# Kernel optimization log

Hardware: AMD Instinct MI355X
Metric: run time of the kernel (lower is better)

## Reference

```python
import jax, jax.numpy as jnp
import numpy as np

# SigNet forward: time-augment -> depth-3 path signature (basepoint=True, via
# Chen's identity over per-segment tensor exponentials) -> Linear. dropout p=0.

B, L, CIN, OUT = 256, 256, 8, 128
C = CIN + 1                      # +1 time channel from signatory.Augment
SIG_CH = C + C**2 + C**3         # signatory.signature_channels(C, depth=3) = 819


def setup_inputs() -> dict:
    key = jax.random.key(0)
    k1, k2, k3 = jax.random.split(key, 3)
    inp = jax.random.normal(k1, (B, L, CIN), dtype=jnp.float32)
    W = jax.random.normal(k2, (SIG_CH, OUT), dtype=jnp.float32) / np.sqrt(SIG_CH).astype(np.float32)
    b = jax.random.normal(k3, (OUT,), dtype=jnp.float32) * 0.01
    return {"inp": inp, "W": W, "b": b}


def _chen(a, bb):
    # Chen's identity for truncated tensor algebra (depth 3):
    # (a*b)_k = sum_{i+j=k} a_i (x) b_j  (with a_0 = b_0 = 1)
    a1, a2, a3 = a
    b1, b2, b3 = bb
    c1 = a1 + b1
    c2 = a2 + b2 + jnp.einsum('...i,...j->...ij', a1, b1)
    c3 = (a3 + b3
          + jnp.einsum('...ij,...k->...ijk', a2, b1)
          + jnp.einsum('...i,...jk->...ijk', a1, b2))
    return (c1, c2, c3)


def _signature_depth3(path):
    # path: [B, L, C]; basepoint=True -> prepend the zero point before diffing
    Bn, Ln, Cn = path.shape
    path = jnp.concatenate([jnp.zeros((Bn, 1, Cn), path.dtype), path], axis=1)
    dx = jnp.moveaxis(jnp.diff(path, axis=1), 1, 0)  # [L, B, C] increments
    # Tensor exponential of each linear segment: exp(dx)_k = dx^{(x)k} / k!
    e1 = dx
    e2 = 0.5 * jnp.einsum('lbi,lbj->lbij', dx, dx)
    e3 = jnp.einsum('lbij,lbk->lbijk', e2, dx) / 3.0  # = dx^(x)3 / 6
    s1, s2, s3 = jax.lax.associative_scan(_chen, (e1, e2, e3), axis=0)
    return jnp.concatenate([s1[-1].reshape(Bn, -1),
                            s2[-1].reshape(Bn, -1),
                            s3[-1].reshape(Bn, -1)], axis=-1)  # [B, SIG_CH]


def reference(inp, W, b):
    Bn, Ln, _ = inp.shape
    # signatory.Augment include_time: linspace(0,1,L) channel, placed first
    t = jnp.broadcast_to(jnp.linspace(0.0, 1.0, Ln, dtype=inp.dtype)[None, :, None], (Bn, Ln, 1))
    x = jnp.concatenate([t, inp], axis=-1)  # [B, L, C]
    y = _signature_depth3(x)
    return y @ W + b  # dropout p=0 is identity
```

## Files before the change

kernel.cpp:

```cpp
#include <hip/hip_runtime.h>


#define ROWF   260
#define NCHUNK 16
#define TPC    27
#define ASTRIDE 29
#define PART_S2_OFF (NCHUNK * TPC * ASTRIDE)
#define UNION_FLOATS (PART_S2_OFF + NCHUNK * 81)

__global__ __launch_bounds__(512) void signet_fwd(
    const float* __restrict__ inp,
    const float* __restrict__ Wg,
    const float* __restrict__ bias,
    float* __restrict__ out)
{
    __shared__ float sig[820];
    __shared__ __align__(16) float u[UNION_FLOATS];

    float* Wt = u;
    float* Dt = u + 9 * ROWF;

    const int tid = threadIdx.x;
    const int b   = blockIdx.x;

    {
        const int t = tid & 255;
        const float* rc = inp + (size_t)b * 2048 + (size_t)t * 8;
        if (tid < 256) {
            float4 c0 = *(const float4*)rc;
            float4 p0 = make_float4(0.f, 0.f, 0.f, 0.f);
            float  tp = 0.f;
            if (t > 0) { p0 = *(const float4*)(rc - 8); tp = (float)(t - 1) * (1.0f / 255.0f); }
            float cur[5] = { (float)t * (1.0f / 255.0f), c0.x, c0.y, c0.z, c0.w };
            float prv[5] = { tp, p0.x, p0.y, p0.z, p0.w };
            #pragma unroll
            for (int c = 0; c < 5; ++c) {
                const float d = cur[c] - prv[c];
                Dt[c * ROWF + t] = d;
                Wt[c * ROWF + t] = prv[c] + 0.5f * d;
            }
        } else {
            float4 c1 = *(const float4*)(rc + 4);
            float4 p1 = make_float4(0.f, 0.f, 0.f, 0.f);
            if (t > 0) p1 = *(const float4*)(rc - 4);
            float cur[4] = { c1.x, c1.y, c1.z, c1.w };
            float prv[4] = { p1.x, p1.y, p1.z, p1.w };
            #pragma unroll
            for (int c = 0; c < 4; ++c) {
                const float d = cur[c] - prv[c];
                Dt[(5 + c) * ROWF + t] = d;
                Wt[(5 + c) * ROWF + t] = prv[c] + 0.5f * d;
            }
        }
    }
    __syncthreads();

    const int  chunk = tid / TPC;
    const int  tloc  = tid - chunk * TPC;
    const int  ci    = tloc / 3;
    const int  kt    = tloc - ci * 3;
    const bool act   = (chunk < NCHUNK);

    float a[9][3];
    float s2a[9];
    #pragma unroll
    for (int j = 0; j < 9; ++j) { s2a[j] = 0.f; a[j][0] = 0.f; a[j][1] = 0.f; a[j][2] = 0.f; }

    if (act) {
        const int fb = chunk * 4;
        const float4* W4 = (const float4*)u;
        const float4* D4 = (const float4*)u + 9 * 65;
        const int k0 = 3 * kt;

        #pragma unroll
        for (int q = 0; q < 4; ++q) {
            const float4 w  = W4[ci * 65 + fb + q];
            const float4 di = D4[ci * 65 + fb + q];
            const float4 Wk0 = W4[(k0 + 0) * 65 + fb + q];
            const float4 Wk1 = W4[(k0 + 1) * 65 + fb + q];
            const float4 Wk2 = W4[(k0 + 2) * 65 + fb + q];
            const float4 Dk0 = D4[(k0 + 0) * 65 + fb + q];
            const float4 Dk1 = D4[(k0 + 1) * 65 + fb + q];
            const float4 Dk2 = D4[(k0 + 2) * 65 + fb + q];

            float4 z, X0, X1, X2;
            z.x = fmaf(-(1.0f / 12.0f), di.x, 0.5f * w.x);
            z.y = fmaf(-(1.0f / 12.0f), di.y, 0.5f * w.y);
            z.z = fmaf(-(1.0f / 12.0f), di.z, 0.5f * w.z);
            z.w = fmaf(-(1.0f / 12.0f), di.w, 0.5f * w.w);
            X0.x = fmaf(0.5f, Dk0.x, Wk0.x); X0.y = fmaf(0.5f, Dk0.y, Wk0.y);
            X0.z = fmaf(0.5f, Dk0.z, Wk0.z); X0.w = fmaf(0.5f, Dk0.w, Wk0.w);
            X1.x = fmaf(0.5f, Dk1.x, Wk1.x); X1.y = fmaf(0.5f, Dk1.y, Wk1.y);
            X1.z = fmaf(0.5f, Dk1.z, Wk1.z); X1.w = fmaf(0.5f, Dk1.w, Wk1.w);
            X2.x = fmaf(0.5f, Dk2.x, Wk2.x); X2.y = fmaf(0.5f, Dk2.y, Wk2.y);
            X2.z = fmaf(0.5f, Dk2.z, Wk2.z); X2.w = fmaf(0.5f, Dk2.w, Wk2.w);

            #pragma unroll
            for (int j = 0; j < 9; ++j) {
                const float4 dj = D4[j * 65 + fb + q];
                { const float uu = w.x * dj.x, vv = z.x * dj.x; s2a[j] += uu;
                  a[j][0] = fmaf(vv, Dk0.x, fmaf(-uu, X0.x, a[j][0]));
                  a[j][1] = fmaf(vv, Dk1.x, fmaf(-uu, X1.x, a[j][1]));
                  a[j][2] = fmaf(vv, Dk2.x, fmaf(-uu, X2.x, a[j][2])); }
                { const float uu = w.y * dj.y, vv = z.y * dj.y; s2a[j] += uu;
                  a[j][0] = fmaf(vv, Dk0.y, fmaf(-uu, X0.y, a[j][0]));
                  a[j][1] = fmaf(vv, Dk1.y, fmaf(-uu, X1.y, a[j][1]));
                  a[j][2] = fmaf(vv, Dk2.y, fmaf(-uu, X2.y, a[j][2])); }
                { const float uu = w.z * dj.z, vv = z.z * dj.z; s2a[j] += uu;
                  a[j][0] = fmaf(vv, Dk0.z, fmaf(-uu, X0.z, a[j][0]));
                  a[j][1] = fmaf(vv, Dk1.z, fmaf(-uu, X1.z, a[j][1]));
                  a[j][2] = fmaf(vv, Dk2.z, fmaf(-uu, X2.z, a[j][2])); }
                { const float uu = w.w * dj.w, vv = z.w * dj.w; s2a[j] += uu;
                  a[j][0] = fmaf(vv, Dk0.w, fmaf(-uu, X0.w, a[j][0]));
                  a[j][1] = fmaf(vv, Dk1.w, fmaf(-uu, X1.w, a[j][1]));
                  a[j][2] = fmaf(vv, Dk2.w, fmaf(-uu, X2.w, a[j][2])); }
            }
        }
    }
    __syncthreads();

    if (tid < 9) {
        const float wl = Wt[tid * ROWF + 255];
        const float dl = Dt[tid * ROWF + 255];
        sig[tid] = fmaf(0.5f, dl, wl);
    }
    __syncthreads();

    if (act) {
        float* pa = u + (chunk * TPC + tloc) * ASTRIDE;
        #pragma unroll
        for (int j = 0; j < 9; ++j) {
            pa[j * 3 + 0] = a[j][0];
            pa[j * 3 + 1] = a[j][1];
            pa[j * 3 + 2] = a[j][2];
        }
        if (kt == 0) {
            float* ps = u + PART_S2_OFF + chunk * 81 + ci * 9;
            #pragma unroll
            for (int j = 0; j < 9; ++j) ps[j] = s2a[j];
        }
    }
    __syncthreads();

    if (tid < 81) {
        float s = 0.f;
        #pragma unroll
        for (int c = 0; c < NCHUNK; ++c) s += u[PART_S2_OFF + c * 81 + tid];
        sig[9 + tid] = s;
    }
    __syncthreads();

    for (int e = tid; e < 729; e += 512) {
        const int i  = e / 81;
        const int r  = e - i * 81;
        const int j  = r / 9;
        const int k  = r - j * 9;
        const int ktv = k / 3;
        const int km  = k - ktv * 3;
        const int toff = (i * 3 + ktv) * ASTRIDE + j * 3 + km;
        float s = 0.f;
        #pragma unroll
        for (int c = 0; c < NCHUNK; ++c) s += u[c * (TPC * ASTRIDE) + toff];
        s = fmaf(sig[9 + i * 9 + j], sig[k], s);
        sig[90 + e] = s;
    }
    __syncthreads();

    {
        const int oq = tid & 31;
        const int sl = tid >> 5;
        float4 acc = make_float4(0.f, 0.f, 0.f, 0.f);
        const float4* Wq = (const float4*)Wg;
        for (int ch = sl; ch < 819; ch += 16) {
            const float s = sig[ch];
            const float4 wv = Wq[(size_t)ch * 32 + oq];
            acc.x = fmaf(s, wv.x, acc.x);
            acc.y = fmaf(s, wv.y, acc.y);
            acc.z = fmaf(s, wv.z, acc.z);
            acc.w = fmaf(s, wv.w, acc.w);
        }
        float4* pbuf = (float4*)u;
        pbuf[sl * 32 + oq] = acc;
    }
    __syncthreads();
    if (tid < 32) {
        const float4* pbuf = (const float4*)u;
        float4 r = pbuf[tid];
        #pragma unroll
        for (int s = 1; s < 16; ++s) {
            const float4 p = pbuf[s * 32 + tid];
            r.x += p.x; r.y += p.y; r.z += p.z; r.w += p.w;
        }
        const float4 bv = ((const float4*)bias)[tid];
        r.x += bv.x; r.y += bv.y; r.z += bv.z; r.w += bv.w;
        ((float4*)(out + (size_t)b * 128))[tid] = r;
    }
}

extern "C" void kernel_launch(void* const* d_in, const int* in_sizes, int n_in,
                              void* d_out, int out_size, void* d_ws, size_t ws_size,
                              hipStream_t stream) {
    const float* inp  = (const float*)d_in[0];
    const float* Wp   = (const float*)d_in[1];
    const float* bias = (const float*)d_in[2];
    float* outp = (float*)d_out;
    (void)in_sizes; (void)n_in; (void)out_size; (void)d_ws; (void)ws_size;

    hipLaunchKernelGGL(signet_fwd, dim3(256), dim3(512), 0, stream,
                       inp, Wp, bias, outp);
}
```

Measured before the change: 18.25 us.

## Split signature across two time segments and two output halves via workspace

The single fused kernel becomes two kernels. The first processes each batch row's path in two halves of 128 steps, one block per half, and writes partial level-2 and level-3 sums to a workspace. The second combines the two partials, adds the level-1 outer-product term, and computes the linear layer with each block covering half of the 128 outputs. The goal is to double the block count from 256 to 512 so more of the device's compute units are busy. The cost is an extra kernel launch, a workspace round trip, and recomputing the signature combine in both output-half blocks.

```diff
diff --git a/kernel.cpp b/kernel.cpp
--- a/kernel.cpp
+++ b/kernel.cpp
@@ -1,55 +1,56 @@
 #include <hip/hip_runtime.h>
 
 
-#define ROWF   260
-#define NCHUNK 16
-#define TPC    27
+#define ROWF    132
+#define NCHUNK  16
+#define TPC     27
 #define ASTRIDE 29
-#define PART_S2_OFF (NCHUNK * TPC * ASTRIDE)
-#define UNION_FLOATS (PART_S2_OFF + NCHUNK * 81)
-
-__global__ __launch_bounds__(512) void signet_fwd(
+#define DUMPF   (NCHUNK * TPC * ASTRIDE)
+#define U1SZ    (DUMPF + NCHUNK * 81)
+#define WSSTR   812
+
+__global__ __launch_bounds__(512) void signet_part(
     const float* __restrict__ inp,
-    const float* __restrict__ Wg,
-    const float* __restrict__ bias,
-    float* __restrict__ out)
+    float* __restrict__ ws)
 {
-    __shared__ float sig[820];
-    __shared__ __align__(16) float u[UNION_FLOATS];
+    __shared__ __align__(16) float u[U1SZ];
+
+    const int tid = threadIdx.x;
+    const int blk = blockIdx.x;
+    const int b   = blk >> 1;
+    const int seg = blk & 1;
 
     float* Wt = u;
     float* Dt = u + 9 * ROWF;
 
-    const int tid = threadIdx.x;
-    const int b   = blockIdx.x;
-
     {
-        const int t = tid & 255;
-        const float* rc = inp + (size_t)b * 2048 + (size_t)t * 8;
-        if (tid < 256) {
+        const int col = tid & 127;
+        const int gt  = seg * 128 + col;
+        const float* rc = inp + (size_t)b * 2048 + (size_t)gt * 8;
+        if (tid < 128) {
             float4 c0 = *(const float4*)rc;
             float4 p0 = make_float4(0.f, 0.f, 0.f, 0.f);
             float  tp = 0.f;
-            if (t > 0) { p0 = *(const float4*)(rc - 8); tp = (float)(t - 1) * (1.0f / 255.0f); }
-            float cur[5] = { (float)t * (1.0f / 255.0f), c0.x, c0.y, c0.z, c0.w };
+            if (gt > 0) { p0 = *(const float4*)(rc - 8); tp = (float)(gt - 1) * (1.0f / 255.0f); }
+            float cur[5] = { (float)gt * (1.0f / 255.0f), c0.x, c0.y, c0.z, c0.w };
             float prv[5] = { tp, p0.x, p0.y, p0.z, p0.w };
             #pragma unroll
             for (int c = 0; c < 5; ++c) {
                 const float d = cur[c] - prv[c];
-                Dt[c * ROWF + t] = d;
-                Wt[c * ROWF + t] = prv[c] + 0.5f * d;
+                Dt[c * ROWF + col] = d;
+                Wt[c * ROWF + col] = prv[c] + 0.5f * d;
             }
-        } else {
+        } else if (tid < 256) {
             float4 c1 = *(const float4*)(rc + 4);
             float4 p1 = make_float4(0.f, 0.f, 0.f, 0.f);
-            if (t > 0) p1 = *(const float4*)(rc - 4);
+            if (gt > 0) p1 = *(const float4*)(rc - 4);
             float cur[4] = { c1.x, c1.y, c1.z, c1.w };
             float prv[4] = { p1.x, p1.y, p1.z, p1.w };
             #pragma unroll
             for (int c = 0; c < 4; ++c) {
                 const float d = cur[c] - prv[c];
-                Dt[(5 + c) * ROWF + t] = d;
-                Wt[(5 + c) * ROWF + t] = prv[c] + 0.5f * d;
+                Dt[(5 + c) * ROWF + col] = d;
+                Wt[(5 + c) * ROWF + col] = prv[c] + 0.5f * d;
             }
         }
     }
@@ -67,21 +68,22 @@
     for (int j = 0; j < 9; ++j) { s2a[j] = 0.f; a[j][0] = 0.f; a[j][1] = 0.f; a[j][2] = 0.f; }
 
     if (act) {
-        const int fb = chunk * 4;
         const float4* W4 = (const float4*)u;
-        const float4* D4 = (const float4*)u + 9 * 65;
+        const float4* D4 = (const float4*)u + 9 * 33;
         const int k0 = 3 * kt;
-
-        #pragma unroll
-        for (int q = 0; q < 4; ++q) {
-            const float4 w  = W4[ci * 65 + fb + q];
-            const float4 di = D4[ci * 65 + fb + q];
-            const float4 Wk0 = W4[(k0 + 0) * 65 + fb + q];
-            const float4 Wk1 = W4[(k0 + 1) * 65 + fb + q];
-            const float4 Wk2 = W4[(k0 + 2) * 65 + fb + q];
-            const float4 Dk0 = D4[(k0 + 0) * 65 + fb + q];
-            const float4 Dk1 = D4[(k0 + 1) * 65 + fb + q];
-            const float4 Dk2 = D4[(k0 + 2) * 65 + fb + q];
+        const int fb = chunk * 2;
+
+        #pragma unroll
+        for (int q = 0; q < 2; ++q) {
+            const int idx = fb + q;
+            const float4 w   = W4[ci * 33 + idx];
+            const float4 di  = D4[ci * 33 + idx];
+            const float4 Wk0 = W4[(k0 + 0) * 33 + idx];
+            const float4 Wk1 = W4[(k0 + 1) * 33 + idx];
+            const float4 Wk2 = W4[(k0 + 2) * 33 + idx];
+            const float4 Dk0 = D4[(k0 + 0) * 33 + idx];
+            const float4 Dk1 = D4[(k0 + 1) * 33 + idx];
+            const float4 Dk2 = D4[(k0 + 2) * 33 + idx];
 
             float4 z, X0, X1, X2;
             z.x = fmaf(-(1.0f / 12.0f), di.x, 0.5f * w.x);
@@ -97,7 +99,7 @@
 
             #pragma unroll
             for (int j = 0; j < 9; ++j) {
-                const float4 dj = D4[j * 65 + fb + q];
+                const float4 dj = D4[j * 33 + idx];
                 { const float uu = w.x * dj.x, vv = z.x * dj.x; s2a[j] += uu;
                   a[j][0] = fmaf(vv, Dk0.x, fmaf(-uu, X0.x, a[j][0]));
                   a[j][1] = fmaf(vv, Dk1.x, fmaf(-uu, X1.x, a[j][1]));
@@ -119,15 +121,8 @@
     }
     __syncthreads();
 
-    if (tid < 9) {
-        const float wl = Wt[tid * ROWF + 255];
-        const float dl = Dt[tid * ROWF + 255];
-        sig[tid] = fmaf(0.5f, dl, wl);
-    }
-    __syncthreads();
-
     if (act) {
-        float* pa = u + (chunk * TPC + tloc) * ASTRIDE;
+        float* pa = u + tid * ASTRIDE;
         #pragma unroll
         for (int j = 0; j < 9; ++j) {
             pa[j * 3 + 0] = a[j][0];
@@ -135,65 +130,93 @@
             pa[j * 3 + 2] = a[j][2];
         }
         if (kt == 0) {
-            float* ps = u + PART_S2_OFF + chunk * 81 + ci * 9;
+            float* ps = u + DUMPF + chunk * 81 + ci * 9;
             #pragma unroll
             for (int j = 0; j < 9; ++j) ps[j] = s2a[j];
         }
     }
     __syncthreads();
 
+    float* wrow = ws + (size_t)blk * WSSTR;
     if (tid < 81) {
         float s = 0.f;
         #pragma unroll
-        for (int c = 0; c < NCHUNK; ++c) s += u[PART_S2_OFF + c * 81 + tid];
-        sig[9 + tid] = s;
-    }
-    __syncthreads();
-
+        for (int c = 0; c < NCHUNK; ++c) s += u[DUMPF + c * 81 + tid];
+        wrow[tid] = s;
+    }
     for (int e = tid; e < 729; e += 512) {
-        const int i  = e / 81;
-        const int r  = e - i * 81;
-        const int j  = r / 9;
-        const int k  = r - j * 9;
+        const int i   = e / 81;
+        const int r   = e - i * 81;
+        const int j   = r / 9;
+        const int k   = r - j * 9;
         const int ktv = k / 3;
         const int km  = k - ktv * 3;
         const int toff = (i * 3 + ktv) * ASTRIDE + j * 3 + km;
         float s = 0.f;
         #pragma unroll
         for (int c = 0; c < NCHUNK; ++c) s += u[c * (TPC * ASTRIDE) + toff];
-        s = fmaf(sig[9 + i * 9 + j], sig[k], s);
-        sig[90 + e] = s;
+        wrow[81 + e] = s;
+    }
+}
+
+__global__ __launch_bounds__(512) void signet_fin(
+    const float* __restrict__ inp,
+    const float* __restrict__ ws,
+    const float* __restrict__ Wg,
+    const float* __restrict__ bias,
+    float* __restrict__ out)
+{
+    __shared__ float sig[820];
+    __shared__ __align__(16) float4 pbuf[32][16];
+
+    const int tid = threadIdx.x;
+    const int b   = blockIdx.x >> 1;
+    const int h   = blockIdx.x & 1;
+
+    const float* pa = ws + (size_t)(2 * b) * WSSTR;
+    const float* pb = pa + WSSTR;
+
+    if (tid < 81) sig[9 + tid] = pa[tid] + pb[tid];
+    if (tid < 9)  sig[tid] = (tid == 0) ? 1.0f
+                             : inp[(size_t)b * 2048 + 255 * 8 + (tid - 1)];
+    __syncthreads();
+
+    for (int e = tid; e < 729; e += 512) {
+        const int i = e / 81;
+        const int r = e - i * 81;
+        const int j = r / 9;
+        const int k = r - j * 9;
+        sig[90 + e] = pa[81 + e] + pb[81 + e] + sig[9 + i * 9 + j] * sig[k];
     }
     __syncthreads();
 
     {
-        const int oq = tid & 31;
-        const int sl = tid >> 5;
+        const int oq = tid & 15;
+        const int sl = tid >> 4;
+        const int cb = h * 16 + oq;
         float4 acc = make_float4(0.f, 0.f, 0.f, 0.f);
         const float4* Wq = (const float4*)Wg;
-        for (int ch = sl; ch < 819; ch += 16) {
+        for (int ch = sl; ch < 819; ch += 32) {
             const float s = sig[ch];
-            const float4 wv = Wq[(size_t)ch * 32 + oq];
+            const float4 wv = Wq[(size_t)ch * 32 + cb];
             acc.x = fmaf(s, wv.x, acc.x);
             acc.y = fmaf(s, wv.y, acc.y);
             acc.z = fmaf(s, wv.z, acc.z);
             acc.w = fmaf(s, wv.w, acc.w);
         }
-        float4* pbuf = (float4*)u;
-        pbuf[sl * 32 + oq] = acc;
-    }
-    __syncthreads();
-    if (tid < 32) {
-        const float4* pbuf = (const float4*)u;
-        float4 r = pbuf[tid];
-        #pragma unroll
-        for (int s = 1; s < 16; ++s) {
-            const float4 p = pbuf[s * 32 + tid];
+        pbuf[sl][oq] = acc;
+    }
+    __syncthreads();
+    if (tid < 16) {
+        float4 r = pbuf[0][tid];
+        #pragma unroll
+        for (int s = 1; s < 32; ++s) {
+            const float4 p = pbuf[s][tid];
             r.x += p.x; r.y += p.y; r.z += p.z; r.w += p.w;
         }
-        const float4 bv = ((const float4*)bias)[tid];
+        const float4 bv = ((const float4*)bias)[h * 16 + tid];
         r.x += bv.x; r.y += bv.y; r.z += bv.z; r.w += bv.w;
-        ((float4*)(out + (size_t)b * 128))[tid] = r;
+        ((float4*)(out + (size_t)b * 128 + h * 64))[tid] = r;
     }
 }
 
@@ -204,8 +227,10 @@
     const float* Wp   = (const float*)d_in[1];
     const float* bias = (const float*)d_in[2];
     float* outp = (float*)d_out;
-    (void)in_sizes; (void)n_in; (void)out_size; (void)d_ws; (void)ws_size;
-
-    hipLaunchKernelGGL(signet_fwd, dim3(256), dim3(512), 0, stream,
-                       inp, Wp, bias, outp);
+    float* wsp  = (float*)d_ws;
+    (void)in_sizes; (void)n_in; (void)out_size; (void)ws_size;
+
+    hipLaunchKernelGGL(signet_part, dim3(512), dim3(512), 0, stream, inp, wsp);
+    hipLaunchKernelGGL(signet_fin,  dim3(512), dim3(512), 0, stream,
+                       inp, wsp, Wp, bias, outp);
 }
```

New measurement: 20.91 us. 1.15x slower.
